# Optimization experiments

Measured on AMD Instinct MI355X. Metric: run time of the kernel, lower is better.

## Reference

```python
import jax, jax.numpy as jnp
import numpy as np

N, K, D, G = 6000, 300, 1024, 16
DG = D // G          # 64 per-head dim
EMB = 64             # position embedding feat_dim


def setup_inputs():
    key = jax.random.key(0)
    ks = jax.random.split(key, 8)
    merged_feat = jax.random.normal(ks[0], (N, D), dtype=jnp.float32)
    u = jax.random.uniform(ks[1], (N, 4), dtype=jnp.float32)
    x1 = u[:, 0] * 800.0
    y1 = u[:, 1] * 800.0
    bboxes = jnp.stack([x1, y1, x1 + u[:, 2] * 200.0 + 8.0, y1 + u[:, 3] * 200.0 + 8.0], axis=1)
    s = 0.02
    Wq = jax.random.normal(ks[2], (D, D), dtype=jnp.float32) * s
    Wk = jax.random.normal(ks[3], (D, D), dtype=jnp.float32) * s
    Wg = jax.random.normal(ks[4], (G, EMB), dtype=jnp.float32) * s
    Wv = jax.random.normal(ks[5], (G, DG, D), dtype=jnp.float32) * s
    bq = jnp.zeros((D,), jnp.float32)
    bk = jnp.zeros((D,), jnp.float32)
    bg = jnp.zeros((G,), jnp.float32)
    bv = jnp.zeros((D,), jnp.float32)
    return dict(merged_feat=merged_feat, bboxes=bboxes, Wq=Wq, bq=bq, Wk=Wk, bk=bk,
                Wg=Wg, bg=bg, Wv=Wv, bv=bv, k=K)


def _cdist(x, y):
    # torch.cdist(p=2): sqrt of clamped squared distances
    sq = jnp.sum(x * x, 1)[:, None] + jnp.sum(y * y, 1)[None, :] - 2.0 * (x @ y.T)
    return jnp.sqrt(jnp.maximum(sq, 0.0))


def _fps_greedy(feat, k):
    # select_farthest_k_sequential: greedy lowest-redundancy sampling on 1/cdist
    Drec = 1.0 / _cdist(feat, feat)  # diagonal -> inf, never argmin-selected

    def step(ds, _):
        idx = jnp.argmin(ds)
        return ds + Drec[idx], idx

    _, rest = jax.lax.scan(step, Drec[0], None, length=k - 1)
    return jnp.concatenate([jnp.zeros((1,), rest.dtype), rest])


def _pos_embedding(bbox, ref_bbox):
    # extract_position_matrix + extract_position_embedding(feat_dim=64)
    xmin, ymin, xmax, ymax = jnp.split(ref_bbox, 4, axis=1)
    wr = xmax - xmin + 1.0
    hr = ymax - ymin + 1.0
    cxr = 0.5 * (xmin + xmax)
    cyr = 0.5 * (ymin + ymax)
    xmin, ymin, xmax, ymax = jnp.split(bbox, 4, axis=1)
    w = xmax - xmin + 1.0
    h = ymax - ymin + 1.0
    cx = 0.5 * (xmin + xmax)
    cy = 0.5 * (ymin + ymax)
    dx = jnp.log(jnp.abs((cx - cxr.T) / w) + 1e-3)
    dy = jnp.log(jnp.abs((cy - cyr.T) / h) + 1e-3)
    dw = jnp.log(w / wr.T)
    dh = jnp.log(h / hr.T)
    pos = jnp.stack([dx, dy, dw, dh], axis=2)            # (k, N, 4)
    rng = jnp.arange(EMB // 8, dtype=jnp.float32)         # 8 frequencies
    dim_mat = jnp.power(1000.0, (8.0 / EMB) * rng)        # (8,)
    div = pos[..., None] * 100.0 / dim_mat               # (k, N, 4, 8)
    emb = jnp.concatenate([jnp.sin(div), jnp.cos(div)], axis=3)  # (k, N, 4, 16)
    return emb.reshape(emb.shape[0], emb.shape[1], EMB)   # (k, N, 64)


def _attention(roi_feat, ref_feat, pos_emb, Wq, bq, Wk, bk, Wg, bg, Wv, bv):
    # attention_module_multi_head: position-gated multi-head relation attention
    k = roi_feat.shape[0]
    # Wgs 1x1 conv (64 -> 16 groups), relu, -> aff_weight (k, G, N)
    aff_weight = jax.nn.relu(jnp.einsum('ge,kne->kgn', Wg, pos_emb) + bg[None, :, None])
    q = (roi_feat @ Wq.T + bq).reshape(k, G, DG)          # (k, G, 64)
    kk = (ref_feat @ Wk.T + bk).reshape(-1, G, DG)        # (N, G, 64)
    aff = jnp.einsum('kgd,ngd->kgn', q, kk) * (1.0 / np.sqrt(float(DG)))
    weighted = jnp.log(aff_weight + 1e-6) + aff
    soft = jax.nn.softmax(weighted, axis=2)               # (k, G, N)
    out_t = jnp.einsum('kgn,nd->kgd', soft, ref_feat)     # (k, G, D)
    # Wvs grouped 1x1 conv (G*D -> D, groups=G)
    return jnp.einsum('kgc,goc->kgo', out_t, Wv).reshape(k, D) + bv


def reference(merged_feat, bboxes, Wq, bq, Wk, bk, Wg, bg, Wv, bv, k):
    idx = _fps_greedy(merged_feat, k)
    roi_feat = merged_feat[idx]
    pos_emb = _pos_embedding(bboxes[idx], bboxes)
    return _attention(roi_feat, merged_feat, pos_emb, Wq, bq, Wk, bk, Wg, bg, Wv, bv)
```

## Files before the change

kernel.cpp:

```cpp
#include <hip/hip_runtime.h>
#include <math.h>

#define N_PTS 6000
#define DIM   1024
#define KSEL  300
#define GG    16
#define DGR   64
#define WSTR  6016
#define XSTR  2048

typedef _Float16 half8 __attribute__((ext_vector_type(8)));
typedef float floatx4 __attribute__((ext_vector_type(4)));

__device__ __forceinline__ unsigned short f2h(float x) {
    _Float16 h = (_Float16)x;
    return __builtin_bit_cast(unsigned short, h);
}
__device__ __forceinline__ float h2f(unsigned short u) {
    return (float)__builtin_bit_cast(_Float16, u);
}

__device__ __forceinline__ void async_copy16(const void* gsrc, void* ldst) {
    __builtin_amdgcn_global_load_lds(
        (const __attribute__((address_space(1))) void*)gsrc,
        (__attribute__((address_space(3))) void*)ldst,
        16, 0, 0);
}

template<bool GRAM, bool OF16>
__global__ __launch_bounds__(256)
void mfma_gemm(const void* Av, long lda, long az,
               const void* Bv, long ldb, long bz,
               void* Cv, long ldc, long cz,
               int M, int N, int Kd,
               const float* __restrict__ bias, long biasz,
               float scale, const float* __restrict__ sqn, int nbm)
{
    __shared__ unsigned short As[128 * 32];
    __shared__ unsigned short Bs[128 * 32];
    const int t = threadIdx.x;
    const int w = t >> 6, l = t & 63;
    const int wr = w >> 1, wc = w & 1;

    int row0, col0, bi = 0, bj = 0;
    if (GRAM) {
        int tt = blockIdx.x, rem = nbm;
        while (tt >= rem) { tt -= rem; bi++; rem--; }
        bj = bi + tt;
        row0 = bi * 128; col0 = bj * 128;
    } else {
        row0 = blockIdx.y * 128; col0 = blockIdx.x * 128;
    }
    const int z = blockIdx.z;
    const unsigned short* Ab = (const unsigned short*)Av + (long)z * az;
    const unsigned short* Bb = (const unsigned short*)Bv + (long)z * bz;

    floatx4 acc[4][4];
#pragma unroll
    for (int i = 0; i < 4; i++)
#pragma unroll
        for (int j = 0; j < 4; j++) acc[i][j] = (floatx4){0.f, 0.f, 0.f, 0.f};

    int ra0 = row0 + (w * 2 + 0) * 16 + (l >> 2); ra0 = ra0 < M ? ra0 : M - 1;
    int ra1 = row0 + (w * 2 + 1) * 16 + (l >> 2); ra1 = ra1 < M ? ra1 : M - 1;
    int rb0 = col0 + (w * 2 + 0) * 16 + (l >> 2); rb0 = rb0 < N ? rb0 : N - 1;
    int rb1 = col0 + (w * 2 + 1) * 16 + (l >> 2); rb1 = rb1 < N ? rb1 : N - 1;
    const long lane_off = (l & 3) * 8;
    const unsigned short* gA0 = Ab + (long)ra0 * lda + lane_off;
    const unsigned short* gA1 = Ab + (long)ra1 * lda + lane_off;
    const unsigned short* gB0 = Bb + (long)rb0 * ldb + lane_off;
    const unsigned short* gB1 = Bb + (long)rb1 * ldb + lane_off;
    unsigned short* lA0 = As + ((w * 2 + 0) * 16) * 32;
    unsigned short* lA1 = As + ((w * 2 + 1) * 16) * 32;
    unsigned short* lB0 = Bs + ((w * 2 + 0) * 16) * 32;
    unsigned short* lB1 = Bs + ((w * 2 + 1) * 16) * 32;

    auto kstep = [&](long offA, long offB) {
        async_copy16(gA0 + offA, (void*)lA0);
        async_copy16(gA1 + offA, (void*)lA1);
        async_copy16(gB0 + offB, (void*)lB0);
        async_copy16(gB1 + offB, (void*)lB1);
        __syncthreads();
        half8 af[4], bfr[4];
#pragma unroll
        for (int ti = 0; ti < 4; ti++)
            af[ti] = *(const half8*)(As + (wr * 64 + ti * 16 + (l & 15)) * 32 + (l >> 4) * 8);
#pragma unroll
        for (int tj = 0; tj < 4; tj++)
            bfr[tj] = *(const half8*)(Bs + (wc * 64 + tj * 16 + (l & 15)) * 32 + (l >> 4) * 8);
#pragma unroll
        for (int ti = 0; ti < 4; ti++)
#pragma unroll
            for (int tj = 0; tj < 4; tj++)
                acc[ti][tj] = __builtin_amdgcn_mfma_f32_16x16x32_f16(
                    af[ti], bfr[tj], acc[ti][tj], 0, 0, 0);
        __syncthreads();
    };

    if (GRAM) {
#pragma unroll 1
        for (int k0 = 0; k0 < 1024; k0 += 32) kstep(k0, k0);
#pragma unroll 1
        for (int k0 = 0; k0 < 1024; k0 += 32) kstep(k0, k0 + 1024);
#pragma unroll 1
        for (int k0 = 0; k0 < 1024; k0 += 32) kstep(k0 + 1024, k0);
    } else {
#pragma unroll 1
        for (int k0 = 0; k0 < Kd; k0 += 32) kstep(k0, k0);
    }

    float* Cf = (float*)Cv + (long)z * cz;
    unsigned short* Ch = (unsigned short*)Cv + (long)z * cz;
    const float* bias_p = bias ? bias + (long)z * biasz : nullptr;
#pragma unroll
    for (int ti = 0; ti < 4; ti++) {
#pragma unroll
        for (int tj = 0; tj < 4; tj++) {
            const int c = col0 + wc * 64 + tj * 16 + (l & 15);
            const int rb = row0 + wr * 64 + ti * 16 + (l >> 4) * 4;
            if (GRAM) {
                float rec4[4];
#pragma unroll
                for (int reg = 0; reg < 4; reg++) {
                    int r = rb + reg;
                    if (r >= M || c >= N) { rec4[reg] = 0.f; continue; }
                    if (r == c) { rec4[reg] = INFINITY; }
                    else {
                        float sq = sqn[r] + sqn[c] - 2.f * acc[ti][tj][reg];
                        rec4[reg] = 1.0f / sqrtf(fmaxf(sq, 0.f));
                    }
                    Cf[(long)r * ldc + c] = rec4[reg];
                }
                if (bi != bj && c < N && rb + 3 < M) {
                    *(float4*)(Cf + (long)c * ldc + rb) =
                        make_float4(rec4[0], rec4[1], rec4[2], rec4[3]);
                }
            } else {
#pragma unroll
                for (int reg = 0; reg < 4; reg++) {
                    int r = rb + reg;
                    if (r >= M || c >= N) continue;
                    float v = acc[ti][tj][reg] * scale;
                    if (bias_p) v += bias_p[c];
                    if (OF16) Ch[(long)r * ldc + c] = f2h(v);
                    else      Cf[(long)r * ldc + c] = v;
                }
            }
        }
    }
}

#define BM 128
#define BN 128
#define BKK 8
#define TM 8
#define TN 8

template<bool TRANSB>
__global__ __launch_bounds__(256)
void sgemm_kernel(const float* __restrict__ A, long lda, long az,
                  const float* __restrict__ B, long ldb, long bz,
                  float* __restrict__ C, long ldc, long cz,
                  int M, int N, int Kd,
                  const float* __restrict__ bias, long biasz, float scale)
{
    __shared__ float As[BKK][BM];
    __shared__ float Bs[BKK][BN];
    const int t = threadIdx.x;
    const int z = blockIdx.z;
    A += (long)z * az; B += (long)z * bz; C += (long)z * cz;
    const float* bias_p = bias ? (bias + (long)z * biasz) : nullptr;
    const int row0 = blockIdx.y * BM;
    const int col0 = blockIdx.x * BN;
    const int tx = t & 15, ty = t >> 4;

    float acc[TM][TN];
#pragma unroll
    for (int i = 0; i < TM; i++)
#pragma unroll
        for (int j = 0; j < TN; j++) acc[i][j] = 0.f;

    const int lrow = t >> 1;
    const int lcol = (t & 1) * 4;

    for (int k0 = 0; k0 < Kd; k0 += BKK) {
        {
            int r = row0 + lrow; r = (r < M) ? r : (M - 1);
            float4 v = *(const float4*)(A + (long)r * lda + (k0 + lcol));
            As[lcol + 0][lrow] = v.x; As[lcol + 1][lrow] = v.y;
            As[lcol + 2][lrow] = v.z; As[lcol + 3][lrow] = v.w;
        }
        {
            int r = col0 + lrow; r = (r < N) ? r : (N - 1);
            float4 v = *(const float4*)(B + (long)r * ldb + (k0 + lcol));
            Bs[lcol + 0][lrow] = v.x; Bs[lcol + 1][lrow] = v.y;
            Bs[lcol + 2][lrow] = v.z; Bs[lcol + 3][lrow] = v.w;
        }
        __syncthreads();
#pragma unroll
        for (int kk = 0; kk < BKK; kk++) {
            float a[TM], b[TN];
#pragma unroll
            for (int i = 0; i < TM; i++) a[i] = As[kk][ty * TM + i];
#pragma unroll
            for (int j = 0; j < TN; j++) b[j] = Bs[kk][tx * TN + j];
#pragma unroll
            for (int i = 0; i < TM; i++)
#pragma unroll
                for (int j = 0; j < TN; j++)
                    acc[i][j] = fmaf(a[i], b[j], acc[i][j]);
        }
        __syncthreads();
    }
#pragma unroll
    for (int i = 0; i < TM; i++) {
        int r = row0 + ty * TM + i;
        if (r >= M) continue;
#pragma unroll
        for (int j = 0; j < TN; j++) {
            int c = col0 + tx * TN + j;
            if (c >= N) continue;
            float v = acc[i][j] * scale;
            if (bias_p) v += bias_p[c];
            C[(long)r * ldc + c] = v;
        }
    }
}

__global__ __launch_bounds__(256)
void sqnpack2_kernel(const float* __restrict__ feat,
                     unsigned short* __restrict__ X, float* __restrict__ sqn)
{
    const int r = blockIdx.x, t = threadIdx.x;
    float4 v = *(const float4*)(feat + (long)r * DIM + t * 4);
    float s = v.x * v.x + v.y * v.y + v.z * v.z + v.w * v.w;

    ushort4 hi, lo;
    hi.x = f2h(v.x); lo.x = f2h(v.x - h2f(hi.x));
    hi.y = f2h(v.y); lo.y = f2h(v.y - h2f(hi.y));
    hi.z = f2h(v.z); lo.z = f2h(v.z - h2f(hi.z));
    hi.w = f2h(v.w); lo.w = f2h(v.w - h2f(hi.w));
    *(ushort4*)(X + (long)r * XSTR + t * 4) = hi;
    *(ushort4*)(X + (long)r * XSTR + 1024 + t * 4) = lo;

#pragma unroll
    for (int o = 32; o > 0; o >>= 1) s += __shfl_down(s, o);
    __shared__ float sr[4];
    if ((t & 63) == 0) sr[t >> 6] = s;
    __syncthreads();
    if (t == 0) sqn[r] = sr[0] + sr[1] + sr[2] + sr[3];
}

__global__ __launch_bounds__(256)
void wconv2_kernel(const float* __restrict__ Wq, const float* __restrict__ Wk,
                   unsigned short* __restrict__ Wq_h, unsigned short* __restrict__ Wk_h)
{
    const int b = blockIdx.x;
    const float* src = (b < 1024) ? Wq : Wk;
    unsigned short* dst = (b < 1024) ? Wq_h : Wk_h;
    const long i = ((long)(b & 1023) * 256 + threadIdx.x) * 4;
    float4 v = *(const float4*)(src + i);
    ushort4 o;
    o.x = f2h(v.x); o.y = f2h(v.y); o.z = f2h(v.z); o.w = f2h(v.w);
    *(ushort4*)(dst + i) = o;
}

__global__ __launch_bounds__(256)
void transpose_kernel(const float* __restrict__ feat, unsigned short* __restrict__ featT)
{
    __shared__ unsigned short tile[32][33];
    const int bx = blockIdx.x;
    const int by = blockIdx.y;
    const int t = threadIdx.x;
    const int lr = t >> 3;
    const int lc = (t & 7) * 4;
    const int r = by * 32 + lr;
    if (r < N_PTS) {
        float4 v = *(const float4*)(feat + (long)r * DIM + bx * 32 + lc);
        tile[lr][lc + 0] = f2h(v.x); tile[lr][lc + 1] = f2h(v.y);
        tile[lr][lc + 2] = f2h(v.z); tile[lr][lc + 3] = f2h(v.w);
    } else {
        tile[lr][lc + 0] = 0; tile[lr][lc + 1] = 0;
        tile[lr][lc + 2] = 0; tile[lr][lc + 3] = 0;
    }
    __syncthreads();
    const int orow = bx * 32 + lr;
    ushort4 o;
    o.x = tile[lc + 0][lr]; o.y = tile[lc + 1][lr];
    o.z = tile[lc + 2][lr]; o.w = tile[lc + 3][lr];
    *(ushort4*)(featT + (long)orow * WSTR + by * 32 + lc) = o;
}

#define FPS_T 1024

__global__ __launch_bounds__(1024)
void fps_kernel(const float* __restrict__ Drec, int* __restrict__ idxout)
{
    const int t = threadIdx.x;
    const bool act = t < 750;
    float ds[8];
    if (act) {
        const float4* p = (const float4*)Drec + 2 * t;
        float4 a0 = p[0], a1 = p[1];
        ds[0] = a0.x; ds[1] = a0.y; ds[2] = a0.z; ds[3] = a0.w;
        ds[4] = a1.x; ds[5] = a1.y; ds[6] = a1.z; ds[7] = a1.w;
    } else {
#pragma unroll
        for (int j = 0; j < 8; j++) ds[j] = INFINITY;
    }
    __shared__ unsigned long long red[16];
    __shared__ int s_sel;
    if (t == 0) idxout[0] = 0;

    for (int it = 1; it < KSEL; it++) {
        float mv = ds[0]; int mi = 8 * t;
#pragma unroll
        for (int j = 1; j < 8; j++) {
            if (ds[j] < mv) { mv = ds[j]; mi = 8 * t + j; }
        }
        unsigned long long key = act
            ? (((unsigned long long)__float_as_uint(mv) << 32) | (unsigned)mi)
            : ~0ull;
#pragma unroll
        for (int o = 32; o > 0; o >>= 1) {
            unsigned long long other = __shfl_down(key, o);
            if (other < key) key = other;
        }
        if ((t & 63) == 0) red[t >> 6] = key;
        __syncthreads();
        if (t < 64) {
            unsigned long long k2 = (t < 16) ? red[t] : ~0ull;
#pragma unroll
            for (int o = 8; o > 0; o >>= 1) {
                unsigned long long other = __shfl_down(k2, o);
                if (other < k2) k2 = other;
            }
            if (t == 0) s_sel = (int)(unsigned)(k2 & 0xffffffffull);
        }
        __syncthreads();
        const int sel = s_sel;
        if (t == 0) idxout[it] = sel;
        if (act) {
            const float4* rp = (const float4*)(Drec + (long)sel * N_PTS) + 2 * t;
            float4 r0 = rp[0], r1 = rp[1];
            ds[0] += r0.x; ds[1] += r0.y; ds[2] += r0.z; ds[3] += r0.w;
            ds[4] += r1.x; ds[5] += r1.y; ds[6] += r1.z; ds[7] += r1.w;
        }
    }
}

__global__ __launch_bounds__(256)
void gatherb_kernel(const unsigned short* __restrict__ X, const int* __restrict__ idx,
                    unsigned short* __restrict__ roi)
{
    const int k = blockIdx.x, t = threadIdx.x;
    const unsigned short* src = X + (long)idx[k] * XSTR;
    *(ushort4*)(roi + (long)k * DIM + t * 4) = *(const ushort4*)(src + t * 4);
}

__global__ __launch_bounds__(256)
void gatesoftmax_kernel(const float* __restrict__ bboxes,
                        const int* __restrict__ idx,
                        const float* __restrict__ Wg,
                        const float* __restrict__ bgp,
                        float* __restrict__ W)
{
    __shared__ float lg[WSTR];
    __shared__ float swg[64];
    __shared__ float sred[4];
    __shared__ float sbb[4];
    __shared__ float sMS;
    const int t = threadIdx.x;
    const int row = blockIdx.x;
    const int k = row >> 4, g = row & 15;
    float* rowp = W + (long)row * WSTR;

    if (t < 64) swg[t] = Wg[g * 64 + t];
    if (t < 4)  sbb[t] = bboxes[(long)idx[k] * 4 + t];
    __syncthreads();

    const float x1 = sbb[0], y1 = sbb[1], x2 = sbb[2], y2 = sbb[3];
    const float w  = x2 - x1 + 1.f, h = y2 - y1 + 1.f;
    const float cx = 0.5f * (x1 + x2), cy = 0.5f * (y1 + y2);
    const float bg_g = bgp[g];
    const float rdm[8] = { 100.0f, 42.169650342858226f, 17.782794100389228f,
                           7.498942093324559f, 3.1622776601683795f,
                           1.333521432163324f, 0.5623413251903491f,
                           0.23713737056616552f };

    float m = -INFINITY;
    for (int n = t; n < N_PTS; n += 256) {
        const float aff = rowp[n];
        float4 rb = *(const float4*)(bboxes + (long)n * 4);
        const float wr = rb.z - rb.x + 1.f, hr = rb.w - rb.y + 1.f;
        const float cxr = 0.5f * (rb.x + rb.z), cyr = 0.5f * (rb.y + rb.w);
        float pos[4];
        pos[0] = __logf(fabsf((cx - cxr) / w) + 1e-3f);
        pos[1] = __logf(fabsf((cy - cyr) / h) + 1e-3f);
        pos[2] = __logf(w / wr);
        pos[3] = __logf(h / hr);
        float gate = bg_g;
#pragma unroll
        for (int p = 0; p < 4; p++) {
#pragma unroll
            for (int f = 0; f < 8; f++) {
                const float arg = pos[p] * rdm[f];
                gate += swg[p * 16 + f] * __sinf(arg)
                      + swg[p * 16 + f + 8] * __cosf(arg);
            }
        }
        const float logit = aff + __logf(fmaxf(gate, 0.f) + 1e-6f);
        lg[n] = logit;
        m = fmaxf(m, logit);
    }
#pragma unroll
    for (int o = 32; o > 0; o >>= 1) m = fmaxf(m, __shfl_down(m, o));
    if ((t & 63) == 0) sred[t >> 6] = m;
    __syncthreads();
    if (t == 0) sMS = fmaxf(fmaxf(sred[0], sred[1]), fmaxf(sred[2], sred[3]));
    __syncthreads();
    m = sMS;
    __syncthreads();

    float s = 0.f;
    for (int n = t; n < N_PTS; n += 256) {
        const float e = __expf(lg[n] - m);
        lg[n] = e;
        s += e;
    }
#pragma unroll
    for (int o = 32; o > 0; o >>= 1) s += __shfl_down(s, o);
    if ((t & 63) == 0) sred[t >> 6] = s;
    __syncthreads();
    if (t == 0) sMS = sred[0] + sred[1] + sred[2] + sred[3];
    __syncthreads();
    const float inv = 1.0f / sMS;
    __syncthreads();

    unsigned short* orow = (unsigned short*)rowp;
    for (int n = t; n < WSTR; n += 256)
        orow[n] = (n < N_PTS) ? f2h(lg[n] * inv) : (unsigned short)0;
}

extern "C" void kernel_launch(void* const* d_in, const int* in_sizes, int n_in,
                              void* d_out, int out_size, void* d_ws, size_t ws_size,
                              hipStream_t stream)
{
    const float* feat   = (const float*)d_in[0];
    const float* bboxes = (const float*)d_in[1];
    const float* Wq     = (const float*)d_in[2];
    const float* bq     = (const float*)d_in[3];
    const float* Wk     = (const float*)d_in[4];
    const float* bk     = (const float*)d_in[5];
    const float* Wg     = (const float*)d_in[6];
    const float* bg     = (const float*)d_in[7];
    const float* Wv     = (const float*)d_in[8];
    const float* bv     = (const float*)d_in[9];
    float* out = (float*)d_out;
    float* ws  = (float*)d_ws;

    float* drec = ws;
    float* W    = ws;
    unsigned short* kk_h  = (unsigned short*)(ws + 28900000);
    unsigned short* q_h   = (unsigned short*)(ws + 31972000);
    unsigned short* roi_h = (unsigned short*)(ws + 32125600);
    unsigned short* featT = (unsigned short*)(ws + 32300000);
    unsigned short* X     = (unsigned short*)(ws + 36000000);
    float* outt           = ws + 36000000;
    unsigned short* Wq_h  = (unsigned short*)(ws + 45216000);
    unsigned short* Wk_h  = (unsigned short*)(ws + 45740288);
    float* sqnbuf         = ws + 46264576;
    int*   idxbuf         = (int*)(ws + 46270576);
    if (ws_size < (size_t)185100000) return;

    sqnpack2_kernel<<<N_PTS, 256, 0, stream>>>(feat, X, sqnbuf);
    wconv2_kernel<<<2048, 256, 0, stream>>>(Wq, Wk, Wq_h, Wk_h);

    mfma_gemm<true, false><<<1128, 256, 0, stream>>>(
        X, XSTR, 0, X, XSTR, 0, drec, N_PTS, 0,
        N_PTS, N_PTS, 3072, nullptr, 0, 1.f, sqnbuf, 47);

    fps_kernel<<<1, FPS_T, 0, stream>>>(drec, idxbuf);

    transpose_kernel<<<dim3(32, 188), 256, 0, stream>>>(feat, featT);
    gatherb_kernel<<<KSEL, 256, 0, stream>>>(X, idxbuf, roi_h);

    mfma_gemm<false, true><<<dim3(8, 3, 1), 256, 0, stream>>>(
        roi_h, 1024, 0, Wq_h, 1024, 0, q_h, 1024, 0,
        KSEL, DIM, DIM, bq, 0, 1.f, nullptr, 0);
    mfma_gemm<false, true><<<dim3(8, 47, 1), 256, 0, stream>>>(
        X, XSTR, 0, Wk_h, 1024, 0, kk_h, 1024, 0,
        N_PTS, DIM, DIM, bk, 0, 1.f, nullptr, 0);

    mfma_gemm<false, false><<<dim3(47, 3, GG), 256, 0, stream>>>(
        q_h, 1024, 64, kk_h, 1024, 64, W, (long)GG * WSTR, WSTR,
        KSEL, N_PTS, 64, nullptr, 0, 0.125f, nullptr, 0);

    gatesoftmax_kernel<<<KSEL * GG, 256, 0, stream>>>(bboxes, idxbuf, Wg, bg, W);

    mfma_gemm<false, false><<<dim3(8, 38, 1), 256, 0, stream>>>(
        (unsigned short*)W, 2 * WSTR, 0, featT, WSTR, 0, outt, DIM, 0,
        KSEL * GG, DIM, WSTR, nullptr, 0, 1.f, nullptr, 0);

    sgemm_kernel<true><<<dim3(1, 3, GG), 256, 0, stream>>>(
        outt, (long)GG * DIM, DIM, Wv, DIM, (long)DGR * DIM, out, DIM, DGR,
        KSEL, DGR, DIM, bv, DGR, 1.f);
}
```

Measured before the change: 1.366 ms.

## Compute position gate once per (k,n) for all heads, split softmax kernel

The fused gate+softmax kernel recomputed the position features and 64 sin/cos per (k,g,n), which is 16x redundant across heads. The change moves gate computation into a separate kernel that computes the sin/cos once per (k,n) and accumulates all 16 head gates, adding the log-gate into W in place. A separate softmax kernel then normalises each row. This cuts the transcendental work 16-fold but adds one extra read-modify-write pass over the 300x16x6000 logit buffer and one more launch.

```diff
diff --git a/kernel.cpp b/kernel.cpp
--- a/kernel.cpp
+++ b/kernel.cpp
@@ -359,59 +359,78 @@
 }
 
 __global__ __launch_bounds__(256)
-void gatesoftmax_kernel(const float* __restrict__ bboxes,
-                        const int* __restrict__ idx,
-                        const float* __restrict__ Wg,
-                        const float* __restrict__ bgp,
-                        float* __restrict__ W)
-{
-    __shared__ float lg[WSTR];
-    __shared__ float swg[64];
-    __shared__ float sred[4];
+void gatelogit_kernel(const float* __restrict__ bboxes,
+                      const int* __restrict__ idx,
+                      const float* __restrict__ Wg,
+                      const float* __restrict__ bgp,
+                      float* __restrict__ W)
+{
+    __shared__ float swg[GG][64];
+    __shared__ float sbg[GG];
     __shared__ float sbb[4];
-    __shared__ float sMS;
     const int t = threadIdx.x;
-    const int row = blockIdx.x;
-    const int k = row >> 4, g = row & 15;
-    float* rowp = W + (long)row * WSTR;
-
-    if (t < 64) swg[t] = Wg[g * 64 + t];
+    const int k = blockIdx.y;
+    const int n = blockIdx.x * 256 + t;
+    for (int i = t; i < GG * 64; i += 256) swg[i >> 6][i & 63] = Wg[i];
+    if (t < GG) sbg[t] = bgp[t];
     if (t < 4)  sbb[t] = bboxes[(long)idx[k] * 4 + t];
     __syncthreads();
+    if (n >= N_PTS) return;
 
     const float x1 = sbb[0], y1 = sbb[1], x2 = sbb[2], y2 = sbb[3];
     const float w  = x2 - x1 + 1.f, h = y2 - y1 + 1.f;
     const float cx = 0.5f * (x1 + x2), cy = 0.5f * (y1 + y2);
-    const float bg_g = bgp[g];
+    float4 rb = *(const float4*)(bboxes + (long)n * 4);
+    const float wr = rb.z - rb.x + 1.f, hr = rb.w - rb.y + 1.f;
+    const float cxr = 0.5f * (rb.x + rb.z), cyr = 0.5f * (rb.y + rb.w);
+
+    float pos[4];
+    pos[0] = __logf(fabsf((cx - cxr) / w) + 1e-3f);
+    pos[1] = __logf(fabsf((cy - cyr) / h) + 1e-3f);
+    pos[2] = __logf(w / wr);
+    pos[3] = __logf(h / hr);
+
     const float rdm[8] = { 100.0f, 42.169650342858226f, 17.782794100389228f,
                            7.498942093324559f, 3.1622776601683795f,
                            1.333521432163324f, 0.5623413251903491f,
                            0.23713737056616552f };
+    float aw[GG];
+#pragma unroll
+    for (int g = 0; g < GG; g++) aw[g] = sbg[g];
+#pragma unroll
+    for (int p = 0; p < 4; p++) {
+#pragma unroll
+        for (int f = 0; f < 8; f++) {
+            const float arg = pos[p] * rdm[f];
+            const float s_ = __sinf(arg), c_ = __cosf(arg);
+            const int e = p * 16 + f;
+#pragma unroll
+            for (int g = 0; g < GG; g++)
+                aw[g] += swg[g][e] * s_ + swg[g][e + 8] * c_;
+        }
+    }
+    float* base = W + ((long)k * GG) * WSTR + n;
+#pragma unroll
+    for (int g = 0; g < GG; g++) {
+        const float lg = __logf(fmaxf(aw[g], 0.f) + 1e-6f);
+        base[(long)g * WSTR] += lg;
+    }
+}
+
+__global__ __launch_bounds__(256)
+void softmax16_kernel(float* __restrict__ W)
+{
+    __shared__ float lg[WSTR];
+    __shared__ float sred[4];
+    __shared__ float sMS;
+    const int t = threadIdx.x;
+    float* rowp = W + (long)blockIdx.x * WSTR;
 
     float m = -INFINITY;
     for (int n = t; n < N_PTS; n += 256) {
-        const float aff = rowp[n];
-        float4 rb = *(const float4*)(bboxes + (long)n * 4);
-        const float wr = rb.z - rb.x + 1.f, hr = rb.w - rb.y + 1.f;
-        const float cxr = 0.5f * (rb.x + rb.z), cyr = 0.5f * (rb.y + rb.w);
-        float pos[4];
-        pos[0] = __logf(fabsf((cx - cxr) / w) + 1e-3f);
-        pos[1] = __logf(fabsf((cy - cyr) / h) + 1e-3f);
-        pos[2] = __logf(w / wr);
-        pos[3] = __logf(h / hr);
-        float gate = bg_g;
-#pragma unroll
-        for (int p = 0; p < 4; p++) {
-#pragma unroll
-            for (int f = 0; f < 8; f++) {
-                const float arg = pos[p] * rdm[f];
-                gate += swg[p * 16 + f] * __sinf(arg)
-                      + swg[p * 16 + f + 8] * __cosf(arg);
-            }
-        }
-        const float logit = aff + __logf(fmaxf(gate, 0.f) + 1e-6f);
-        lg[n] = logit;
-        m = fmaxf(m, logit);
+        const float v = rowp[n];
+        lg[n] = v;
+        m = fmaxf(m, v);
     }
 #pragma unroll
     for (int o = 32; o > 0; o >>= 1) m = fmaxf(m, __shfl_down(m, o));
@@ -496,7 +515,9 @@
         q_h, 1024, 64, kk_h, 1024, 64, W, (long)GG * WSTR, WSTR,
         KSEL, N_PTS, 64, nullptr, 0, 0.125f, nullptr, 0);
 
-    gatesoftmax_kernel<<<KSEL * GG, 256, 0, stream>>>(bboxes, idxbuf, Wg, bg, W);
+    gatelogit_kernel<<<dim3(24, KSEL), 256, 0, stream>>>(
+        bboxes, idxbuf, Wg, bg, W);
+    softmax16_kernel<<<KSEL * GG, 256, 0, stream>>>(W);
 
     mfma_gemm<false, false><<<dim3(8, 38, 1), 256, 0, stream>>>(
         (unsigned short*)W, 2 * WSTR, 0, featT, WSTR, 0, outt, DIM, 0,
```

Measured after the change: 1.227 ms. -10.2%, faster.
